# Performance work log

Hardware: AMD Instinct MI355X
Metric: run time of the kernel (lower is better)

The kernel has to match this reference:

```python
import jax, jax.numpy as jnp
import numpy as np

B, T, D_MODEL, NHEAD, D_HEAD = 8, 4096, 1024, 16, 64


def setup_inputs() -> dict:
    key = jax.random.key(0)
    ks = jax.random.split(key, 8)
    return {
        "inputs": jax.random.normal(ks[0], (B, T, D_MODEL), jnp.float32),
        "z0": jax.random.normal(ks[1], (NHEAD, D_HEAD), jnp.float32),
        "W_in": jax.random.normal(ks[2], (D_MODEL, D_MODEL), jnp.float32) / np.sqrt(D_MODEL),
        "b_in": jax.random.normal(ks[3], (D_MODEL,), jnp.float32) * 0.01,
        "W_out": jax.random.normal(ks[4], (D_MODEL, D_MODEL), jnp.float32) / np.sqrt(D_MODEL),
        "b_out": jax.random.normal(ks[5], (D_MODEL,), jnp.float32) * 0.01,
        "smoothing_logit": jax.random.normal(ks[6], (NHEAD, 1), jnp.float32),
        "v0": jax.random.normal(ks[7], (1, 1, NHEAD, D_HEAD), jnp.float32),
    }


def reference(inputs, z0, W_in, b_in, W_out, b_out, smoothing_logit, v0):
    b, t, d = inputs.shape
    nhead, d_head = z0.shape
    # in projection -> (b, t, h, d_head)
    values = (inputs @ W_in + b_in).reshape(b, t, nhead, d_head)
    # prepend learned z0, then temporal differencing -> (b, t, h, d_head)
    z0_b = jnp.broadcast_to(z0[None, None], (b, 1, nhead, d_head))
    values = jnp.concatenate([z0_b, values], axis=1)
    values = values[:, 1:] - values[:, :-1]
    # exponential smoothing recurrence: s_j = a*s_{j-1} + (1-a)*v_j, s_{-1} = v0
    alpha = jax.nn.sigmoid(smoothing_logit)           # (h, 1)
    a = alpha[None]                                   # (1, h, 1) broadcast over batch
    s0 = jnp.broadcast_to(v0[0, 0][None], (b, nhead, d_head))

    def step(s, v):                                   # v: (b, h, d_head)
        s = a * s + (1.0 - a) * v
        return s, s

    _, es_out = jax.lax.scan(step, s0, jnp.swapaxes(values, 0, 1))  # (t, b, h, d)
    es_out = jnp.swapaxes(es_out, 0, 1)               # (b, t, h, d_head)
    # prepend v0 -> length t+1
    v0_b = jnp.broadcast_to(v0, (b, 1, nhead, d_head))
    out = jnp.concatenate([v0_b, es_out], axis=1)     # (b, t+1, h, d_head)
    out = out.reshape(b, t + 1, nhead * d_head)
    return out @ W_out + b_out                        # (b, t+1, d_model)
```

## Files before the change

### kernel.cpp

```cpp
#include <hip/hip_runtime.h>
#include <hip/hip_bf16.h>
#include <stdint.h>

#define DEV static __device__ __forceinline__

typedef __attribute__((ext_vector_type(8))) short bf16x8;
typedef __attribute__((ext_vector_type(4))) float f32x4;
typedef unsigned int u32;

static constexpr int T = 4096;
static constexpr int BATCH = 8;
static constexpr int DM = 1024;
static constexpr int M1 = BATCH * T;
static constexpr int M2 = BATCH * (T + 1);
static constexpr int M2P = 129 * 256;
static constexpr int NCH = 64;
static constexpr int CL = T / NCH;
static constexpr int NT = 32;

DEV unsigned short f2bf(float f) {
  union { float f; unsigned u; } v; v.f = f;
  unsigned u = v.u;
  return (unsigned short)((u + 0x7fffu + ((u >> 16) & 1u)) >> 16);
}
DEV float bf2f(unsigned short s) {
  union { unsigned u; float f; } v; v.u = ((unsigned)s) << 16;
  return v.f;
}

DEV void gl_lds16(const unsigned short* g, unsigned short* lds) {
  __builtin_amdgcn_global_load_lds(
      (const __attribute__((address_space(1))) u32*)g,
      (__attribute__((address_space(3))) u32*)lds,
      16, 0, 0);
}

__global__ void k_cvt_x(const float4* __restrict__ x, ushort4* __restrict__ o) {
  int i = blockIdx.x * 256 + threadIdx.x;
  float4 v = x[i];
  ushort4 r;
  r.x = f2bf(v.x); r.y = f2bf(v.y); r.z = f2bf(v.z); r.w = f2bf(v.w);
  o[i] = r;
}

__global__ void k_transpose(const float* __restrict__ w0, const float* __restrict__ w1,
                            unsigned short* __restrict__ t0, unsigned short* __restrict__ t1) {
  __shared__ float tile[32][33];
  const float* src = blockIdx.z ? w1 : w0;
  unsigned short* dst = blockIdx.z ? t1 : t0;
  int bx = blockIdx.x * 32;
  int by = blockIdx.y * 32;
  int tx = threadIdx.x & 31, ty = threadIdx.x >> 5;
#pragma unroll
  for (int r = 0; r < 32; r += 8)
    tile[ty + r][tx] = src[(by + ty + r) * DM + bx + tx];
  __syncthreads();
#pragma unroll
  for (int r = 0; r < 32; r += 8)
    dst[(bx + ty + r) * DM + by + tx] = f2bf(tile[tx][ty + r]);
}

template <int MODE>
__global__ __launch_bounds__(512, 2) void k_gemm(const unsigned short* __restrict__ A16,
                                                 const unsigned short* __restrict__ Bt16,
                                                 const float* __restrict__ bias,
                                                 unsigned short* __restrict__ outb,
                                                 float* __restrict__ outf, int Mvalid) {
  __shared__ unsigned short lds[4 * 16384];

  const int tid = threadIdx.x;
  const int w = tid >> 6, l = tid & 63;
  const int wm = w >> 2, wn = w & 3;
  const int rr = l & 15, kg = l >> 4;

  const int nwg = gridDim.x, orig = blockIdx.x;
  const int q = nwg >> 3, r8 = nwg & 7;
  const int xcd = orig & 7, idx = orig >> 3;
  const int wg = (xcd < r8 ? xcd * (q + 1) : r8 * (q + 1) + (xcd - r8) * q) + idx;
  const int bm = wg >> 2, bn = wg & 3;
  const int blockM = bm * 256;
  const int blockN = bn * 256;

  f32x4 acc[8][4];
#pragma unroll
  for (int m = 0; m < 8; m++)
#pragma unroll
    for (int n = 0; n < 4; n++) acc[m][n] = (f32x4){0.f, 0.f, 0.f, 0.f};

  const unsigned short* pA[2];
  const unsigned short* pB[2];
#pragma unroll
  for (int cc = 0; cc < 2; cc++) {
    int rp = w * 32 + cc * 16 + (l >> 2);
    int sl = (l & 3) ^ ((rp >> 1) & 3);
    pA[cc] = A16 + (size_t)(blockM + rp) * DM + sl * 8;
    pB[cc] = Bt16 + (size_t)(blockN + rp) * DM + sl * 8;
  }

  int offA[8], offB[4];
#pragma unroll
  for (int mf = 0; mf < 8; mf++) {
    int rrow = wm * 128 + mf * 16 + rr;
    offA[mf] = rrow * 32 + ((kg ^ ((rrow >> 1) & 3)) * 8);
  }
#pragma unroll
  for (int nf = 0; nf < 4; nf++) {
    int rb = wn * 64 + nf * 16 + rr;
    offB[nf] = 8192 + rb * 32 + ((kg ^ ((rb >> 1) & 3)) * 8);
  }

  auto stageA = [&](int t) {
    unsigned short* d = lds + (t & 3) * 16384 + w * 1024;
#pragma unroll
    for (int cc = 0; cc < 2; cc++) gl_lds16(pA[cc] + (size_t)t * 32, d + cc * 512);
  };
  auto stageB = [&](int t) {
    unsigned short* d = lds + (t & 3) * 16384 + 8192 + w * 1024;
#pragma unroll
    for (int cc = 0; cc < 2; cc++) gl_lds16(pB[cc] + (size_t)t * 32, d + cc * 512);
  };

  stageA(0); stageB(0);
  stageA(1); stageB(1);
  stageA(2); stageB(2);

  for (int t = 0; t < NT; ++t) {
    if (t < NT - 2)       asm volatile("s_waitcnt vmcnt(8)" ::: "memory");
    else if (t == NT - 2) asm volatile("s_waitcnt vmcnt(4)" ::: "memory");
    else                  asm volatile("s_waitcnt vmcnt(0)" ::: "memory");
    __builtin_amdgcn_s_barrier();
    asm volatile("" ::: "memory");

    const unsigned short* buf = lds + (t & 3) * 16384;
    const bool do_stage = (t + 3 < NT);

    bf16x8 bq[4], aq[4];
#pragma unroll
    for (int nf = 0; nf < 4; nf++) bq[nf] = *(const bf16x8*)(buf + offB[nf]);
#pragma unroll
    for (int mf = 0; mf < 4; mf++) aq[mf] = *(const bf16x8*)(buf + offA[mf]);
    if (do_stage) stageA(t + 3);
    __builtin_amdgcn_s_setprio(1);
#pragma unroll
    for (int mf = 0; mf < 4; mf++)
#pragma unroll
      for (int nf = 0; nf < 4; nf++)
        acc[mf][nf] = __builtin_amdgcn_mfma_f32_16x16x32_bf16(aq[mf], bq[nf], acc[mf][nf], 0, 0, 0);
    __builtin_amdgcn_s_setprio(0);
    __builtin_amdgcn_s_barrier();

#pragma unroll
    for (int mf = 0; mf < 4; mf++) aq[mf] = *(const bf16x8*)(buf + offA[4 + mf]);
    if (do_stage) stageB(t + 3);
    __builtin_amdgcn_s_setprio(1);
#pragma unroll
    for (int mf = 0; mf < 4; mf++)
#pragma unroll
      for (int nf = 0; nf < 4; nf++)
        acc[4 + mf][nf] = __builtin_amdgcn_mfma_f32_16x16x32_bf16(aq[mf], bq[nf], acc[4 + mf][nf], 0, 0, 0);
    __builtin_amdgcn_s_setprio(0);
  }

#pragma unroll
  for (int nf = 0; nf < 4; nf++) {
    int col = blockN + wn * 64 + nf * 16 + (l & 15);
    float bv = bias[col];
#pragma unroll
    for (int mf = 0; mf < 8; mf++) {
      int row = blockM + wm * 128 + mf * 16 + (l >> 4) * 4;
#pragma unroll
      for (int j = 0; j < 4; j++) {
        float v = acc[mf][nf][j] + bv;
        if (MODE == 0) {
          outb[(size_t)(row + j) * DM + col] = f2bf(v);
        } else {
          if (row + j < Mvalid) outf[(size_t)(row + j) * DM + col] = v;
        }
      }
    }
  }
}

__global__ void k_scan_partial(const unsigned short* __restrict__ proj,
                               const float* __restrict__ logit,
                               const float* __restrict__ z0,
                               float* __restrict__ chunkend) {
  int b = blockIdx.x >> 6, c = blockIdx.x & 63;
  int ch = threadIdx.x;
  float a = 1.f / (1.f + expf(-logit[ch >> 6]));
  int t0 = c * CL;
  const unsigned short* p = proj + (size_t)(b * T + t0) * DM + ch;
  float pprev = (t0 == 0) ? z0[ch] : bf2f(p[-DM]);
  float s = 0.f;
  for (int j = 0; j < CL; j++) {
    float pv = bf2f(p[(size_t)j * DM]);
    s = a * s + (1.f - a) * (pv - pprev);
    pprev = pv;
  }
  chunkend[(b * NCH + c) * DM + ch] = s;
}

__global__ void k_scan_combine(const float* __restrict__ chunkend,
                               const float* __restrict__ logit,
                               const float* __restrict__ v0,
                               float* __restrict__ enter) {
  int b = blockIdx.x;
  int ch = threadIdx.x;
  float a = 1.f / (1.f + expf(-logit[ch >> 6]));
  float a2 = a * a, a4 = a2 * a2, a8 = a4 * a4, a16 = a8 * a8, a32 = a16 * a16;
  float aL = a32 * a32;
  float e = v0[ch];
  enter[(b * NCH + 0) * DM + ch] = e;
  for (int c = 1; c < NCH; c++) {
    e = aL * e + chunkend[(b * NCH + c - 1) * DM + ch];
    enter[(b * NCH + c) * DM + ch] = e;
  }
}

__global__ void k_scan_final(const unsigned short* __restrict__ proj,
                             const float* __restrict__ logit,
                             const float* __restrict__ z0,
                             const float* __restrict__ v0,
                             const float* __restrict__ enter,
                             unsigned short* __restrict__ S) {
  int b = blockIdx.x >> 6, c = blockIdx.x & 63;
  int ch = threadIdx.x;
  float a = 1.f / (1.f + expf(-logit[ch >> 6]));
  int t0 = c * CL;
  const unsigned short* p = proj + (size_t)(b * T + t0) * DM + ch;
  unsigned short* so = S + (size_t)(b * (T + 1) + t0 + 1) * DM + ch;
  float pprev = (t0 == 0) ? z0[ch] : bf2f(p[-DM]);
  float s = enter[(b * NCH + c) * DM + ch];
  if (c == 0) S[(size_t)b * (T + 1) * DM + ch] = f2bf(v0[ch]);
  for (int j = 0; j < CL; j++) {
    float pv = bf2f(p[(size_t)j * DM]);
    s = a * s + (1.f - a) * (pv - pprev);
    pprev = pv;
    so[(size_t)j * DM] = f2bf(s);
  }
}

__global__ void k_pad(unsigned short* __restrict__ S) {
  int i = blockIdx.x * 256 + threadIdx.x;
  if (i < (M2P - M2) * DM) S[(size_t)M2 * DM + i] = 0;
}

extern "C" void kernel_launch(void* const* d_in, const int* in_sizes, int n_in,
                              void* d_out, int out_size, void* d_ws, size_t ws_size,
                              hipStream_t stream) {
  const float* inputs = (const float*)d_in[0];
  const float* z0     = (const float*)d_in[1];
  const float* W_in   = (const float*)d_in[2];
  const float* b_in   = (const float*)d_in[3];
  const float* W_out  = (const float*)d_in[4];
  const float* b_out  = (const float*)d_in[5];
  const float* slogit = (const float*)d_in[6];
  const float* v0     = (const float*)d_in[7];
  float* out = (float*)d_out;

  char* ws = (char*)d_ws;
  unsigned short* X16   = (unsigned short*)(ws);
  unsigned short* P16   = (unsigned short*)(ws + 67108864);
  unsigned short* S16   = (unsigned short*)(ws + 134217728);
  unsigned short* WTin  = (unsigned short*)(ws + 201850880);
  unsigned short* WTout = (unsigned short*)(ws + 203948032);
  float* chunkend       = (float*)(ws + 206045184);
  float* enter          = (float*)(ws + 208142336);

  k_cvt_x<<<32768, 256, 0, stream>>>((const float4*)inputs, (ushort4*)X16);
  k_transpose<<<dim3(32, 32, 2), 256, 0, stream>>>(W_in, W_out, WTin, WTout);
  k_gemm<0><<<dim3((M1 / 256) * 4), 512, 0, stream>>>(X16, WTin, b_in, P16, nullptr, M1);
  k_scan_partial<<<dim3(BATCH * NCH), 1024, 0, stream>>>(P16, slogit, z0, chunkend);
  k_scan_combine<<<dim3(BATCH), 1024, 0, stream>>>(chunkend, slogit, v0, enter);
  k_scan_final<<<dim3(BATCH * NCH), 1024, 0, stream>>>(P16, slogit, z0, v0, enter, S16);
  k_pad<<<dim3(992), 256, 0, stream>>>(S16);
  k_gemm<1><<<dim3((M2P / 256) * 4), 512, 0, stream>>>(S16, WTout, b_out, nullptr, out, M2);
}
```

Before: 301.5 us.

## Fuse fp32-to-bf16 input conversion into GEMM A-load and restructure pipeline

```diff
diff --git a/kernel.cpp b/kernel.cpp
--- a/kernel.cpp
+++ b/kernel.cpp
@@ -16,7 +16,7 @@
 static constexpr int M2P = 129 * 256;
 static constexpr int NCH = 64;
 static constexpr int CL = T / NCH;
-static constexpr int NT = 32;
+static constexpr int NT = 16;
 
 DEV unsigned short f2bf(float f) {
   union { float f; unsigned u; } v; v.f = f;
@@ -27,20 +27,13 @@
   union { unsigned u; float f; } v; v.u = ((unsigned)s) << 16;
   return v.f;
 }
-
-DEV void gl_lds16(const unsigned short* g, unsigned short* lds) {
-  __builtin_amdgcn_global_load_lds(
-      (const __attribute__((address_space(1))) u32*)g,
-      (__attribute__((address_space(3))) u32*)lds,
-      16, 0, 0);
-}
-
-__global__ void k_cvt_x(const float4* __restrict__ x, ushort4* __restrict__ o) {
-  int i = blockIdx.x * 256 + threadIdx.x;
-  float4 v = x[i];
-  ushort4 r;
-  r.x = f2bf(v.x); r.y = f2bf(v.y); r.z = f2bf(v.z); r.w = f2bf(v.w);
-  o[i] = r;
+DEV bf16x8 pack8(float4 a, float4 b) {
+  bf16x8 r;
+  r[0] = (short)f2bf(a.x); r[1] = (short)f2bf(a.y);
+  r[2] = (short)f2bf(a.z); r[3] = (short)f2bf(a.w);
+  r[4] = (short)f2bf(b.x); r[5] = (short)f2bf(b.y);
+  r[6] = (short)f2bf(b.z); r[7] = (short)f2bf(b.w);
+  return r;
 }
 
 __global__ void k_transpose(const float* __restrict__ w0, const float* __restrict__ w1,
@@ -61,121 +54,145 @@
 }
 
 template <int MODE>
-__global__ __launch_bounds__(512, 2) void k_gemm(const unsigned short* __restrict__ A16,
+__global__ __launch_bounds__(512, 2) void k_gemm(const void* __restrict__ Asrc,
                                                  const unsigned short* __restrict__ Bt16,
                                                  const float* __restrict__ bias,
                                                  unsigned short* __restrict__ outb,
                                                  float* __restrict__ outf, int Mvalid) {
-  __shared__ unsigned short lds[4 * 16384];
+  __shared__ unsigned short lds[2 * 16384];
 
   const int tid = threadIdx.x;
   const int w = tid >> 6, l = tid & 63;
   const int wm = w >> 2, wn = w & 3;
-  const int rr = l & 15, kg = l >> 4;
+  const int lo = l & 15, hi = l >> 4;
 
   const int nwg = gridDim.x, orig = blockIdx.x;
-  const int q = nwg >> 3, r8 = nwg & 7;
+  const int q8 = nwg >> 3, r8 = nwg & 7;
   const int xcd = orig & 7, idx = orig >> 3;
-  const int wg = (xcd < r8 ? xcd * (q + 1) : r8 * (q + 1) + (xcd - r8) * q) + idx;
+  const int wg = (xcd < r8 ? xcd * (q8 + 1) : r8 * (q8 + 1) + (xcd - r8) * q8) + idx;
   const int bm = wg >> 2, bn = wg & 3;
   const int blockM = bm * 256;
   const int blockN = bn * 256;
 
+  const float* A32 = (const float*)Asrc;
+  const unsigned short* A16 = (const unsigned short*)Asrc;
+
   f32x4 acc[8][4];
 #pragma unroll
   for (int m = 0; m < 8; m++)
 #pragma unroll
     for (int n = 0; n < 4; n++) acc[m][n] = (f32x4){0.f, 0.f, 0.f, 0.f};
 
-  const unsigned short* pA[2];
-  const unsigned short* pB[2];
-#pragma unroll
-  for (int cc = 0; cc < 2; cc++) {
-    int rp = w * 32 + cc * 16 + (l >> 2);
-    int sl = (l & 3) ^ ((rp >> 1) & 3);
-    pA[cc] = A16 + (size_t)(blockM + rp) * DM + sl * 8;
-    pB[cc] = Bt16 + (size_t)(blockN + rp) * DM + sl * 8;
-  }
-
-  int offA[8], offB[4];
+  const unsigned short* pB = Bt16 + (size_t)(blockN + wn * 64 + lo) * DM + hi * 8;
+
+  const int sr = tid >> 3;
+  const int ss = tid & 7;
+  const int ssw = ss ^ (sr & 7);
+
+  float4 sa[2][2];
+  uint4 sb[2];
+
+  auto loads_half = [&](int tt, int h) {
+#pragma unroll
+    for (int r2 = 0; r2 < 2; r2++) {
+      const int rnd = h * 2 + r2;
+      if (MODE == 0) {
+        const float* p = A32 + (size_t)(blockM + rnd * 64 + sr) * DM + (size_t)tt * 64 + ss * 8;
+        sa[r2][0] = *(const float4*)p;
+        sa[r2][1] = *(const float4*)(p + 4);
+      } else {
+        const unsigned short* p = A16 + (size_t)(blockM + rnd * 64 + sr) * DM + (size_t)tt * 64 + ss * 8;
+        sb[r2] = *(const uint4*)p;
+      }
+    }
+  };
+  auto write_half = [&](int buf, int h) {
+#pragma unroll
+    for (int r2 = 0; r2 < 2; r2++) {
+      const int rnd = h * 2 + r2;
+      unsigned short* d = lds + buf * 16384 + (rnd * 64 + sr) * 64 + ssw * 8;
+      if (MODE == 0) *(bf16x8*)d = pack8(sa[r2][0], sa[r2][1]);
+      else           *(uint4*)d = sb[r2];
+    }
+  };
+
+  bf16x8 bq[2][4][2];
+
+#pragma unroll
+  for (int nf = 0; nf < 4; nf++)
+#pragma unroll
+    for (int kh = 0; kh < 2; kh++)
+      bq[0][nf][kh] = *(const bf16x8*)(pB + (size_t)nf * 16 * DM + kh * 32);
+  loads_half(0, 0);
+  write_half(0, 0);
+  loads_half(0, 1);
+  write_half(0, 1);
+  __builtin_amdgcn_sched_barrier(0);
+  asm volatile("s_waitcnt lgkmcnt(0)");
+  __builtin_amdgcn_sched_barrier(0);
+  __builtin_amdgcn_s_barrier();
+  __builtin_amdgcn_sched_barrier(0);
+
+#define KHBLOCK(CB, KH)                                                       \
+  _Pragma("unroll") for (int mf = 0; mf < 8; mf++) {                          \
+    const int ml = wm * 128 + mf * 16 + lo;                                   \
+    const bf16x8 aq = *(const bf16x8*)(lds + (CB) * 16384 + ml * 64 +         \
+                                       ((((KH) << 2) | hi) ^ (ml & 7)) * 8);  \
+    _Pragma("unroll") for (int nf = 0; nf < 4; nf++)                          \
+      acc[mf][nf] = __builtin_amdgcn_mfma_f32_16x16x32_bf16(                  \
+          bq[CB][nf][KH], aq, acc[mf][nf], 0, 0, 0);                          \
+  }
+
+#define TILE(tt, CB)                                                          \
+  {                                                                           \
+    const bool hasN = (tt) + 1 < NT;                                          \
+    if (hasN) {                                                               \
+      _Pragma("unroll") for (int nf = 0; nf < 4; nf++)                        \
+        _Pragma("unroll") for (int kh = 0; kh < 2; kh++)                      \
+          bq[(CB) ^ 1][nf][kh] = *(const bf16x8*)(pB + (size_t)nf * 16 * DM + \
+                                                  ((tt) + 1) * 64 + kh * 32); \
+      loads_half((tt) + 1, 0);                                                \
+    }                                                                         \
+    KHBLOCK(CB, 0)                                                            \
+    if (hasN) { write_half((CB) ^ 1, 0); loads_half((tt) + 1, 1); }           \
+    KHBLOCK(CB, 1)                                                            \
+    if (hasN) write_half((CB) ^ 1, 1);                                        \
+    __builtin_amdgcn_sched_barrier(0);                                        \
+    asm volatile("s_waitcnt lgkmcnt(0)");                                     \
+    __builtin_amdgcn_sched_barrier(0);                                        \
+    __builtin_amdgcn_s_barrier();                                             \
+    __builtin_amdgcn_sched_barrier(0);                                        \
+  }
+
+  for (int t = 0; t < NT; t += 2) {
+    TILE(t, 0)
+    TILE(t + 1, 1)
+  }
+#undef TILE
+#undef KHBLOCK
+
 #pragma unroll
   for (int mf = 0; mf < 8; mf++) {
-    int rrow = wm * 128 + mf * 16 + rr;
-    offA[mf] = rrow * 32 + ((kg ^ ((rrow >> 1) & 3)) * 8);
-  }
-#pragma unroll
-  for (int nf = 0; nf < 4; nf++) {
-    int rb = wn * 64 + nf * 16 + rr;
-    offB[nf] = 8192 + rb * 32 + ((kg ^ ((rb >> 1) & 3)) * 8);
-  }
-
-  auto stageA = [&](int t) {
-    unsigned short* d = lds + (t & 3) * 16384 + w * 1024;
-#pragma unroll
-    for (int cc = 0; cc < 2; cc++) gl_lds16(pA[cc] + (size_t)t * 32, d + cc * 512);
-  };
-  auto stageB = [&](int t) {
-    unsigned short* d = lds + (t & 3) * 16384 + 8192 + w * 1024;
-#pragma unroll
-    for (int cc = 0; cc < 2; cc++) gl_lds16(pB[cc] + (size_t)t * 32, d + cc * 512);
-  };
-
-  stageA(0); stageB(0);
-  stageA(1); stageB(1);
-  stageA(2); stageB(2);
-
-  for (int t = 0; t < NT; ++t) {
-    if (t < NT - 2)       asm volatile("s_waitcnt vmcnt(8)" ::: "memory");
-    else if (t == NT - 2) asm volatile("s_waitcnt vmcnt(4)" ::: "memory");
-    else                  asm volatile("s_waitcnt vmcnt(0)" ::: "memory");
-    __builtin_amdgcn_s_barrier();
-    asm volatile("" ::: "memory");
-
-    const unsigned short* buf = lds + (t & 3) * 16384;
-    const bool do_stage = (t + 3 < NT);
-
-    bf16x8 bq[4], aq[4];
-#pragma unroll
-    for (int nf = 0; nf < 4; nf++) bq[nf] = *(const bf16x8*)(buf + offB[nf]);
-#pragma unroll
-    for (int mf = 0; mf < 4; mf++) aq[mf] = *(const bf16x8*)(buf + offA[mf]);
-    if (do_stage) stageA(t + 3);
-    __builtin_amdgcn_s_setprio(1);
-#pragma unroll
-    for (int mf = 0; mf < 4; mf++)
-#pragma unroll
-      for (int nf = 0; nf < 4; nf++)
-        acc[mf][nf] = __builtin_amdgcn_mfma_f32_16x16x32_bf16(aq[mf], bq[nf], acc[mf][nf], 0, 0, 0);
-    __builtin_amdgcn_s_setprio(0);
-    __builtin_amdgcn_s_barrier();
-
-#pragma unroll
-    for (int mf = 0; mf < 4; mf++) aq[mf] = *(const bf16x8*)(buf + offA[4 + mf]);
-    if (do_stage) stageB(t + 3);
-    __builtin_amdgcn_s_setprio(1);
-#pragma unroll
-    for (int mf = 0; mf < 4; mf++)
-#pragma unroll
-      for (int nf = 0; nf < 4; nf++)
-        acc[4 + mf][nf] = __builtin_amdgcn_mfma_f32_16x16x32_bf16(aq[mf], bq[nf], acc[4 + mf][nf], 0, 0, 0);
-    __builtin_amdgcn_s_setprio(0);
-  }
-
-#pragma unroll
-  for (int nf = 0; nf < 4; nf++) {
-    int col = blockN + wn * 64 + nf * 16 + (l & 15);
-    float bv = bias[col];
-#pragma unroll
-    for (int mf = 0; mf < 8; mf++) {
-      int row = blockM + wm * 128 + mf * 16 + (l >> 4) * 4;
-#pragma unroll
-      for (int j = 0; j < 4; j++) {
-        float v = acc[mf][nf][j] + bv;
-        if (MODE == 0) {
-          outb[(size_t)(row + j) * DM + col] = f2bf(v);
-        } else {
-          if (row + j < Mvalid) outf[(size_t)(row + j) * DM + col] = v;
-        }
+    const int row = blockM + wm * 128 + mf * 16 + lo;
+    if (MODE == 1 && row >= Mvalid) continue;
+#pragma unroll
+    for (int nf = 0; nf < 4; nf++) {
+      const int col = blockN + wn * 64 + nf * 16 + hi * 4;
+      const float4 bv = *(const float4*)(bias + col);
+      if (MODE == 0) {
+        ushort4 o;
+        o.x = f2bf(acc[mf][nf][0] + bv.x);
+        o.y = f2bf(acc[mf][nf][1] + bv.y);
+        o.z = f2bf(acc[mf][nf][2] + bv.z);
+        o.w = f2bf(acc[mf][nf][3] + bv.w);
+        *(ushort4*)(outb + (size_t)row * DM + col) = o;
+      } else {
+        float4 o;
+        o.x = acc[mf][nf][0] + bv.x;
+        o.y = acc[mf][nf][1] + bv.y;
+        o.z = acc[mf][nf][2] + bv.z;
+        o.w = acc[mf][nf][3] + bv.w;
+        *(float4*)(outf + (size_t)row * DM + col) = o;
       }
     }
   }
@@ -259,17 +276,15 @@
   float* out = (float*)d_out;
 
   char* ws = (char*)d_ws;
-  unsigned short* X16   = (unsigned short*)(ws);
-  unsigned short* P16   = (unsigned short*)(ws + 67108864);
-  unsigned short* S16   = (unsigned short*)(ws + 134217728);
-  unsigned short* WTin  = (unsigned short*)(ws + 201850880);
-  unsigned short* WTout = (unsigned short*)(ws + 203948032);
-  float* chunkend       = (float*)(ws + 206045184);
-  float* enter          = (float*)(ws + 208142336);
-
-  k_cvt_x<<<32768, 256, 0, stream>>>((const float4*)inputs, (ushort4*)X16);
+  unsigned short* P16   = (unsigned short*)(ws);
+  unsigned short* S16   = (unsigned short*)(ws + 67108864);
+  unsigned short* WTin  = (unsigned short*)(ws + 134742016);
+  unsigned short* WTout = (unsigned short*)(ws + 136839168);
+  float* chunkend       = (float*)(ws + 138936320);
+  float* enter          = (float*)(ws + 141033472);
+
   k_transpose<<<dim3(32, 32, 2), 256, 0, stream>>>(W_in, W_out, WTin, WTout);
-  k_gemm<0><<<dim3((M1 / 256) * 4), 512, 0, stream>>>(X16, WTin, b_in, P16, nullptr, M1);
+  k_gemm<0><<<dim3((M1 / 256) * 4), 512, 0, stream>>>(inputs, WTin, b_in, P16, nullptr, M1);
   k_scan_partial<<<dim3(BATCH * NCH), 1024, 0, stream>>>(P16, slogit, z0, chunkend);
   k_scan_combine<<<dim3(BATCH), 1024, 0, stream>>>(chunkend, slogit, v0, enter);
   k_scan_final<<<dim3(BATCH * NCH), 1024, 0, stream>>>(P16, slogit, z0, v0, enter, S16);
```

Measured after the change: 446.4 us. 1.48x slower.
